# Performance work log

Measured on AMD Instinct MI355X. Metric: run time of the kernel, lower is better.

Reference implementation:

```python
import jax, jax.numpy as jnp
import numpy as np

B, T, D, H, DFF = 64, 100, 1024, 16, 4096
HD = D // H
EPS = 1e-5


def _rope_tables(t_len, hd, dtype):
    # matches RotaryEmbedding: inv_freq over even dims, emb = cat([freqs, freqs])
    inv_freq = 1.0 / (10000.0 ** (jnp.arange(0, hd, 2, dtype=jnp.float32) / hd))
    t = jnp.arange(t_len, dtype=jnp.float32)
    freqs = jnp.einsum('i,j->ij', t, inv_freq)          # (T, hd/2)
    emb = jnp.concatenate([freqs, freqs], axis=-1)      # (T, hd)
    # apply_rope uses cos[..., ::2] / sin[..., ::2]
    cos = jnp.cos(emb)[:, ::2].astype(dtype)            # (T, hd/2)
    sin = jnp.sin(emb)[:, ::2].astype(dtype)
    return cos, sin


def _apply_rope(x, cos, sin):
    # x: (B, H, T, hd); cos/sin: (T, hd/2) broadcast over B,H
    x1 = x[..., ::2]
    x2 = x[..., 1::2]
    return jnp.concatenate([x1 * cos - x2 * sin, x1 * sin + x2 * cos], axis=-1)


def _layernorm(x, g, b):
    mu = jnp.mean(x, axis=-1, keepdims=True)
    var = jnp.mean(jnp.square(x - mu), axis=-1, keepdims=True)
    return (x - mu) * jax.lax.rsqrt(var + EPS) * g + b


def setup_inputs() -> dict:
    key = jax.random.key(0)
    ks = jax.random.split(key, 8)
    s = 0.02
    return {
        'tgt': jax.random.normal(ks[0], (B, T, D), dtype=jnp.float32),
        'Wqkv': jax.random.normal(ks[1], (3 * D, D), dtype=jnp.float32) * s,
        'bqkv': jnp.zeros((3 * D,), jnp.float32),
        'Wo': jax.random.normal(ks[2], (D, D), dtype=jnp.float32) * s,
        'bo': jnp.zeros((D,), jnp.float32),
        'W1': jax.random.normal(ks[3], (DFF, D), dtype=jnp.float32) * s,
        'b1': jnp.zeros((DFF,), jnp.float32),
        'W2': jax.random.normal(ks[4], (D, DFF), dtype=jnp.float32) * s,
        'b2': jnp.zeros((D,), jnp.float32),
        'g1': jnp.ones((D,), jnp.float32),
        'be1': jnp.zeros((D,), jnp.float32),
        'g2': jnp.ones((D,), jnp.float32),
        'be2': jnp.zeros((D,), jnp.float32),
        'tgt_mask': jnp.tril(jnp.ones((T, T), jnp.int32)),
    }


def reference(tgt, Wqkv, bqkv, Wo, bo, W1, b1, W2, b2, g1, be1, g2, be2, tgt_mask):
    dtype = tgt.dtype
    # QKV projection (torch Linear: x @ W.T + b)
    qkv = jnp.einsum('btd,ed->bte', tgt, Wqkv) + bqkv          # (B,T,3D)
    qkv = qkv.reshape(B, T, 3, H, HD).transpose(2, 0, 3, 1, 4)  # (3,B,H,T,hd)
    q, k, v = qkv[0], qkv[1], qkv[2]

    cos, sin = _rope_tables(T, HD, dtype)
    q = _apply_rope(q, cos, sin)
    k = _apply_rope(k, cos, sin)

    scale = 1.0 / np.sqrt(HD)
    scores = jnp.einsum('bhqd,bhkd->bhqk', q, k) * scale        # (B,H,T,T)
    scores = jnp.where(tgt_mask == 0, -jnp.inf, scores)
    attn = jax.nn.softmax(scores, axis=-1)
    ctx = jnp.einsum('bhqk,bhkd->bhqd', attn, v)                # (B,H,T,hd)
    ctx = ctx.transpose(0, 2, 1, 3).reshape(B, T, D)

    tgt2 = jnp.einsum('btd,ed->bte', ctx, Wo) + bo
    x = _layernorm(tgt + tgt2, g1, be1)

    h = jax.nn.relu(jnp.einsum('btd,fd->btf', x, W1) + b1)
    ff = jnp.einsum('btf,df->btd', h, W2) + b2
    out = _layernorm(x + ff, g2, be2)
    return out
```

## Files before the change

### kernel.cpp

```cpp
#include <hip/hip_runtime.h>
#include <math.h>

#define Bn   64
#define Tn   100
#define Tp   128
#define Dn   1024
#define Hn   16
#define HDn  64
#define DFFn 4096
#define EPSf 1e-5f

typedef unsigned short ushort_t;
typedef __attribute__((ext_vector_type(8))) __bf16 bf16x8;
typedef __attribute__((ext_vector_type(4))) float f32x4;

__device__ __forceinline__ float u2f(ushort_t u) {
    union { unsigned int i; float f; } v; v.i = ((unsigned int)u) << 16; return v.f;
}
__device__ __forceinline__ ushort_t f2bf(float f) {
    union { float f; unsigned int u; } v; v.f = f;
    unsigned int r = v.u + 0x7FFFu + ((v.u >> 16) & 1u);
    return (ushort_t)(r >> 16);
}

__device__ __forceinline__ void gload_lds16(const void* g, void* l) {
    __builtin_amdgcn_global_load_lds(
        (const __attribute__((address_space(1))) unsigned int*)g,
        (__attribute__((address_space(3))) unsigned int*)l,
        16, 0, 0);
}

struct ConvSeg { const float* src; ushort_t* dst; int n4; };
struct Conv5   { ConvSeg seg[5]; };

__global__ __launch_bounds__(256) void conv_bf16_multi(Conv5 cfg)
{
    int i = blockIdx.x * 256 + threadIdx.x;
    #pragma unroll
    for (int s = 0; s < 5; ++s) {
        const int n = cfg.seg[s].n4;
        if (i < n) {
            float4 v = ((const float4*)cfg.seg[s].src)[i];
            ushort4 o;
            o.x = f2bf(v.x); o.y = f2bf(v.y); o.z = f2bf(v.z); o.w = f2bf(v.w);
            ((ushort4*)cfg.seg[s].dst)[i] = o;
            return;
        }
        i -= n;
    }
}

#define GEMM_TILE_MAP(gx_, gy_)                                              \
    const int L  = blockIdx.x;                                               \
    const int group = L / (8 * (gx_));                                       \
    int l = L - group * 8 * (gx_);                                           \
    const int rem = (gy_) - group * 8;                                       \
    int rowt, colt;                                                          \
    if (rem >= 8) { rowt = group * 8 + (l & 7); colt = l >> 3; }             \
    else          { rowt = group * 8 + l % rem; colt = l / rem; }

#define GEMM_KLOOP(A_, B_, K_)                                               \
    for (int k0 = 0; k0 < (K_); k0 += 64) {                                  \
        __syncthreads();                                                     \
        _Pragma("unroll")                                                    \
        for (int t = 0; t < 4; ++t) {                                        \
            const int idx = (wave * 4 + t) * 64 + lane;                      \
            const int row = idx >> 3;                                        \
            const int gc  = (idx & 7) ^ (row & 7);                           \
            gload_lds16((A_) + (size_t)(row0 + row) * (K_) + k0 + gc * 8,    \
                        &As[idx * 8]);                                       \
            gload_lds16((B_) + (size_t)(col0 + row) * (K_) + k0 + gc * 8,    \
                        &Bs[idx * 8]);                                       \
        }                                                                    \
        __syncthreads();                                                     \
        _Pragma("unroll")                                                    \
        for (int kh = 0; kh < 2; ++kh) {                                     \
            const int chunk = kh * 4 + g;                                    \
            bf16x8 af[4], bfr[4];                                            \
            _Pragma("unroll")                                                \
            for (int i = 0; i < 4; ++i) {                                    \
                const int ra = wrow + i * 16 + frow;                         \
                af[i]  = *(const bf16x8*)&As[ra * 64 + (chunk ^ (ra & 7)) * 8]; \
                const int rb = wcol + i * 16 + frow;                         \
                bfr[i] = *(const bf16x8*)&Bs[rb * 64 + (chunk ^ (rb & 7)) * 8]; \
            }                                                                \
            _Pragma("unroll")                                                \
            for (int i = 0; i < 4; ++i)                                      \
                _Pragma("unroll")                                            \
                for (int j = 0; j < 4; ++j)                                  \
                    acc[i][j] = __builtin_amdgcn_mfma_f32_16x16x32_bf16(     \
                        af[i], bfr[j], acc[i][j], 0, 0, 0);                  \
        }                                                                    \
    }

template<bool RELU, typename OutT>
__global__ __launch_bounds__(256) void gemm_bt_mfma(const ushort_t* __restrict__ A,
                                                    const ushort_t* __restrict__ Bm,
                                                    const float* __restrict__ bias,
                                                    OutT* __restrict__ C,
                                                    int M, int N, int K, int gx)
{
    __shared__ __align__(16) ushort_t As[128 * 64];
    __shared__ __align__(16) ushort_t Bs[128 * 64];

    const int gy = M >> 7;
    GEMM_TILE_MAP(gx, gy)

    const int tid  = threadIdx.x;
    const int wave = tid >> 6;
    const int lane = tid & 63;
    const int row0 = rowt * 128;
    const int col0 = colt * 128;
    const int wrow = (wave >> 1) * 64;
    const int wcol = (wave & 1) * 64;
    const int frow = lane & 15;
    const int g    = lane >> 4;

    f32x4 acc[4][4] = {};
    GEMM_KLOOP(A, Bm, K)

    const int crow = (lane >> 4) * 4;
    const int ccol = lane & 15;
    #pragma unroll
    for (int i = 0; i < 4; ++i) {
        #pragma unroll
        for (int r = 0; r < 4; ++r) {
            const int row = row0 + wrow + i * 16 + crow + r;
            #pragma unroll
            for (int j = 0; j < 4; ++j) {
                const int col = col0 + wcol + j * 16 + ccol;
                float v = acc[i][j][r] + bias[col];
                if (RELU) v = fmaxf(v, 0.f);
                if constexpr (sizeof(OutT) == 2)
                    C[(size_t)row * N + col] = (OutT)f2bf(v);
                else
                    C[(size_t)row * N + col] = (OutT)v;
            }
        }
    }
}

__global__ __launch_bounds__(256) void gemm_qkv_rope(const ushort_t* __restrict__ A,
                                                     const ushort_t* __restrict__ Bm,
                                                     const float* __restrict__ bias,
                                                     ushort_t* __restrict__ q,
                                                     ushort_t* __restrict__ k,
                                                     ushort_t* __restrict__ vt)
{
    __shared__ __align__(16) ushort_t As[128 * 64];
    __shared__ __align__(16) ushort_t Bs[128 * 64];

    const int gy = 50, gx = 24;
    GEMM_TILE_MAP(gx, gy)

    const int tid  = threadIdx.x;
    const int wave = tid >> 6;
    const int lane = tid & 63;
    const int row0 = rowt * 128;
    const int col0 = colt * 128;
    const int wrow = (wave >> 1) * 64;
    const int wcol = (wave & 1) * 64;
    const int frow = lane & 15;
    const int g    = lane >> 4;

    f32x4 acc[4][4] = {};
    GEMM_KLOOP(A, Bm, Dn)

    const int crow = (lane >> 4) * 4;
    const int ccol = lane & 15;
    const int sec  = col0 >> 10;

    if (sec == 2) {
        #pragma unroll
        for (int i = 0; i < 4; ++i) {
            #pragma unroll
            for (int r = 0; r < 4; ++r) {
                const int row = row0 + wrow + i * 16 + crow + r;
                const int b = row / Tn, t = row - b * Tn;
                #pragma unroll
                for (int j = 0; j < 4; ++j) {
                    const int colg = col0 + wcol + j * 16 + ccol;
                    const int hcol = colg & 1023;
                    const int h = hcol >> 6, d = hcol & 63;
                    const float v = acc[i][j][r] + bias[colg];
                    vt[((size_t)(b * Hn + h) * HDn + d) * Tp + t] = f2bf(v);
                }
            }
        }
    } else {
        ushort_t* dst = sec ? k : q;
        const int odd = ccol & 1;
        const float fr0 = exp2f(-0.83048202f * (float)(ccol >> 1));
        const float fr1 = exp2f(-0.83048202f * (float)(8 + (ccol >> 1)));
        #pragma unroll
        for (int i = 0; i < 4; ++i) {
            #pragma unroll
            for (int r = 0; r < 4; ++r) {
                const int row = row0 + wrow + i * 16 + crow + r;
                const int b = row / Tn, t = row - b * Tn;
                float s0, c0, s1, c1;
                sincosf((float)t * fr0, &s0, &c0);
                sincosf((float)t * fr1, &s1, &c1);
                #pragma unroll
                for (int j = 0; j < 4; ++j) {
                    const int colg = col0 + wcol + j * 16 + ccol;
                    const int hcol = colg & 1023;
                    const int h  = hcol >> 6;
                    const int dh = hcol & 63;
                    const int m  = dh >> 1;
                    const float val   = acc[i][j][r] + bias[colg];
                    const float other = __shfl_xor(val, 1);
                    const float sn = (j & 1) ? s1 : s0;
                    const float cs = (j & 1) ? c1 : c0;
                    const float x1 = odd ? other : val;
                    const float x2 = odd ? val : other;
                    const float o  = odd ? (x1 * sn + x2 * cs)
                                         : (x1 * cs - x2 * sn);
                    const int outcol = odd ? (m + 32) : m;
                    dst[((size_t)(b * Hn + h) * Tp + t) * HDn + outcol] = f2bf(o);
                }
            }
        }
    }
}

__global__ __launch_bounds__(256) void attn_mfma(const ushort_t* __restrict__ q,
                                                 const ushort_t* __restrict__ k,
                                                 const ushort_t* __restrict__ vt,
                                                 ushort_t* __restrict__ ctx)
{
    __shared__ __align__(16) ushort_t sm[24576];

    const int bh   = blockIdx.x;
    const int b    = bh >> 4, h = bh & 15;
    const int tid  = threadIdx.x;
    const int wave = tid >> 6;
    const int lane = tid & 63;
    const int c    = lane & 15;
    const int g    = lane >> 4;
    const int R0   = wave * 32;

    const ushort_t* qg = q  + (size_t)bh * Tp * HDn;
    const ushort_t* kg = k  + (size_t)bh * Tp * HDn;
    const ushort_t* vg = vt + (size_t)bh * HDn * Tp;
    for (int s = wave; s < 16; s += 4) {
        const int idx = s * 64 + lane;
        { const int row = idx >> 3, pc = idx & 7, gc = pc ^ (row & 7);
          gload_lds16(qg + row * 64 + gc * 8, &sm[idx * 8]);
          gload_lds16(kg + row * 64 + gc * 8, &sm[8192 + idx * 8]); }
        { const int row = idx >> 4, pc = idx & 15, gc = pc ^ (row & 15);
          gload_lds16(vg + row * 128 + gc * 8, &sm[16384 + idx * 8]); }
    }
    __syncthreads();

    f32x4 acc[2][8] = {};
    #pragma unroll
    for (int ks = 0; ks < 2; ++ks) {
        const int cb = ks * 4;
        bf16x8 aq[2];
        #pragma unroll
        for (int i = 0; i < 2; ++i) {
            const int row = R0 + i * 16 + c;
            const int ph  = (cb + g) ^ (row & 7);
            aq[i] = *(const bf16x8*)&sm[row * 64 + ph * 8];
        }
        #pragma unroll
        for (int j = 0; j < 8; ++j) {
            const int row = j * 16 + c;
            const int ph  = (cb + g) ^ (row & 7);
            const bf16x8 bk = *(const bf16x8*)&sm[8192 + row * 64 + ph * 8];
            acc[0][j] = __builtin_amdgcn_mfma_f32_16x16x32_bf16(aq[0], bk, acc[0][j], 0, 0, 0);
            acc[1][j] = __builtin_amdgcn_mfma_f32_16x16x32_bf16(aq[1], bk, acc[1][j], 0, 0, 0);
        }
    }
    __syncthreads();

    float linv[2][4];
    #pragma unroll
    for (int i = 0; i < 2; ++i) {
        #pragma unroll
        for (int r = 0; r < 4; ++r) {
            const int row = R0 + i * 16 + g * 4 + r;
            float sv[8], m = -1e30f;
            #pragma unroll
            for (int j = 0; j < 8; ++j) {
                const int col = j * 16 + c;
                const float s = acc[i][j][r] * 0.125f;
                sv[j] = (col <= row) ? s : -1e30f;
                m = fmaxf(m, sv[j]);
            }
            #pragma unroll
            for (int msk = 1; msk < 16; msk <<= 1) m = fmaxf(m, __shfl_xor(m, msk));
            float l = 0.f;
            #pragma unroll
            for (int j = 0; j < 8; ++j) {
                const int col = j * 16 + c;
                const float p = (col <= row) ? __expf(sv[j] - m) : 0.f;
                sv[j] = p; l += p;
            }
            #pragma unroll
            for (int msk = 1; msk < 16; msk <<= 1) l += __shfl_xor(l, msk);
            linv[i][r] = 1.f / l;
            #pragma unroll
            for (int j = 0; j < 8; ++j) {
                const int chunk = j * 2 + (c >> 3);
                const int ph    = chunk ^ (row & 15);
                sm[row * 128 + ph * 8 + (c & 7)] = f2bf(sv[j]);
            }
        }
    }
    __syncthreads();

    f32x4 acc2[2][4] = {};
    #pragma unroll
    for (int ks = 0; ks < 4; ++ks) {
        const int cb = ks * 4;
        bf16x8 ap[2];
        #pragma unroll
        for (int i = 0; i < 2; ++i) {
            const int row = R0 + i * 16 + c;
            const int ph  = (cb + g) ^ (row & 15);
            ap[i] = *(const bf16x8*)&sm[row * 128 + ph * 8];
        }
        #pragma unroll
        for (int n = 0; n < 4; ++n) {
            const int row = n * 16 + c;
            const int ph  = (cb + g) ^ (row & 15);
            const bf16x8 bv = *(const bf16x8*)&sm[16384 + row * 128 + ph * 8];
            acc2[0][n] = __builtin_amdgcn_mfma_f32_16x16x32_bf16(ap[0], bv, acc2[0][n], 0, 0, 0);
            acc2[1][n] = __builtin_amdgcn_mfma_f32_16x16x32_bf16(ap[1], bv, acc2[1][n], 0, 0, 0);
        }
    }

    #pragma unroll
    for (int i = 0; i < 2; ++i) {
        #pragma unroll
        for (int r = 0; r < 4; ++r) {
            const int row = R0 + i * 16 + g * 4 + r;
            if (row < Tn) {
                const float s = linv[i][r];
                #pragma unroll
                for (int n = 0; n < 4; ++n) {
                    const int col = n * 16 + c;
                    ctx[(size_t)(b * Tn + row) * Dn + h * HDn + col] =
                        f2bf(acc2[i][n][r] * s);
                }
            }
        }
    }
}

__global__ __launch_bounds__(256) void add_ln1(const float* __restrict__ a,
                                               const ushort_t* __restrict__ r,
                                               const float* __restrict__ g,
                                               const float* __restrict__ be,
                                               ushort_t* __restrict__ out_bf)
{
    const int row = blockIdx.x;
    const int tid = threadIdx.x;
    __shared__ float red[256];
    const size_t base = (size_t)row * Dn;

    float vals[4];
    float s = 0.f;
    #pragma unroll
    for (int i = 0; i < 4; ++i) {
        const int c = tid + i * 256;
        vals[i] = a[base + c] + u2f(r[base + c]);
        s += vals[i];
    }
    red[tid] = s;
    __syncthreads();
    for (int o = 128; o > 0; o >>= 1) {
        if (tid < o) red[tid] += red[tid + o];
        __syncthreads();
    }
    const float mu = red[0] * (1.f / Dn);
    __syncthreads();

    float vs = 0.f;
    #pragma unroll
    for (int i = 0; i < 4; ++i) { const float d = vals[i] - mu; vs += d * d; }
    red[tid] = vs;
    __syncthreads();
    for (int o = 128; o > 0; o >>= 1) {
        if (tid < o) red[tid] += red[tid + o];
        __syncthreads();
    }
    const float rstd = rsqrtf(red[0] * (1.f / Dn) + EPSf);

    #pragma unroll
    for (int i = 0; i < 4; ++i) {
        const int c = tid + i * 256;
        out_bf[base + c] = f2bf((vals[i] - mu) * rstd * g[c] + be[c]);
    }
}

__global__ __launch_bounds__(256) void add_ln2(const ushort_t* __restrict__ a,
                                               const ushort_t* __restrict__ r,
                                               const float* __restrict__ g,
                                               const float* __restrict__ be,
                                               float* __restrict__ out)
{
    const int row = blockIdx.x;
    const int tid = threadIdx.x;
    __shared__ float red[256];
    const size_t base = (size_t)row * Dn;

    float vals[4];
    float s = 0.f;
    #pragma unroll
    for (int i = 0; i < 4; ++i) {
        const int c = tid + i * 256;
        vals[i] = u2f(a[base + c]) + u2f(r[base + c]);
        s += vals[i];
    }
    red[tid] = s;
    __syncthreads();
    for (int o = 128; o > 0; o >>= 1) {
        if (tid < o) red[tid] += red[tid + o];
        __syncthreads();
    }
    const float mu = red[0] * (1.f / Dn);
    __syncthreads();

    float vs = 0.f;
    #pragma unroll
    for (int i = 0; i < 4; ++i) { const float d = vals[i] - mu; vs += d * d; }
    red[tid] = vs;
    __syncthreads();
    for (int o = 128; o > 0; o >>= 1) {
        if (tid < o) red[tid] += red[tid + o];
        __syncthreads();
    }
    const float rstd = rsqrtf(red[0] * (1.f / Dn) + EPSf);

    #pragma unroll
    for (int i = 0; i < 4; ++i) {
        const int c = tid + i * 256;
        out[base + c] = (vals[i] - mu) * rstd * g[c] + be[c];
    }
}

extern "C" void kernel_launch(void* const* d_in, const int* in_sizes, int n_in,
                              void* d_out, int out_size, void* d_ws, size_t ws_size,
                              hipStream_t stream)
{
    const float* tgt  = (const float*)d_in[0];
    const float* Wqkv = (const float*)d_in[1];
    const float* bqkv = (const float*)d_in[2];
    const float* Wo   = (const float*)d_in[3];
    const float* bo   = (const float*)d_in[4];
    const float* W1   = (const float*)d_in[5];
    const float* b1   = (const float*)d_in[6];
    const float* W2   = (const float*)d_in[7];
    const float* b2   = (const float*)d_in[8];
    const float* g1   = (const float*)d_in[9];
    const float* be1  = (const float*)d_in[10];
    const float* g2   = (const float*)d_in[11];
    const float* be2  = (const float*)d_in[12];
    float* out = (float*)d_out;
    (void)in_sizes; (void)n_in; (void)out_size; (void)ws_size;

    const int M = Bn * Tn;

    char* w = (char*)d_ws;
    ushort_t* tgt_bf  = (ushort_t*)(w);
    ushort_t* Wqkv_bf = (ushort_t*)(w + 13107200);
    ushort_t* Wo_bf   = (ushort_t*)(w + 19398656);
    ushort_t* W1_bf   = (ushort_t*)(w + 21495808);
    ushort_t* W2_bf   = (ushort_t*)(w + 29884416);

    ushort_t* qb    = (ushort_t*)(w + 38273024);
    ushort_t* kb    = (ushort_t*)(w + 55050240);
    ushort_t* vtb   = (ushort_t*)(w + 71827456);
    ushort_t* hbuf  = (ushort_t*)(w + 38273024);
    ushort_t* ctxb  = (ushort_t*)(w + 88604672);
    ushort_t* tgt2b = (ushort_t*)(w + 101711872);
    ushort_t* ffb   = (ushort_t*)(w + 101711872);
    ushort_t* x_bf  = (ushort_t*)(w + 114819072);

    Conv5 cfg;
    cfg.seg[0] = { tgt,  tgt_bf,  M * Dn / 4 };
    cfg.seg[1] = { Wqkv, Wqkv_bf, 3 * Dn * Dn / 4 };
    cfg.seg[2] = { Wo,   Wo_bf,   Dn * Dn / 4 };
    cfg.seg[3] = { W1,   W1_bf,   DFFn * Dn / 4 };
    cfg.seg[4] = { W2,   W2_bf,   Dn * DFFn / 4 };
    const int total4 = (M * Dn + 3 * Dn * Dn + Dn * Dn + 2 * DFFn * Dn) / 4;
    conv_bf16_multi<<<(total4 + 255) / 256, 256, 0, stream>>>(cfg);

    gemm_qkv_rope<<<1200, 256, 0, stream>>>(tgt_bf, Wqkv_bf, bqkv, qb, kb, vtb);
    attn_mfma<<<Bn * Hn, 256, 0, stream>>>(qb, kb, vtb, ctxb);
    gemm_bt_mfma<false, ushort_t><<<(Dn / 128) * (M / 128), 256, 0, stream>>>(
        ctxb, Wo_bf, bo, tgt2b, M, Dn, Dn, Dn / 128);
    add_ln1<<<M, 256, 0, stream>>>(tgt, tgt2b, g1, be1, x_bf);
    gemm_bt_mfma<true, ushort_t><<<(DFFn / 128) * (M / 128), 256, 0, stream>>>(
        x_bf, W1_bf, b1, hbuf, M, DFFn, Dn, DFFn / 128);
    gemm_bt_mfma<false, ushort_t><<<(Dn / 128) * (M / 128), 256, 0, stream>>>(
        hbuf, W2_bf, b2, ffb, M, Dn, DFFn, Dn / 128);
    add_ln2<<<M, 256, 0, stream>>>(x_bf, ffb, g2, be2, out);
}
```

Measured before the change: 450.9 us.

## Fuse residual into Wo GEMM, precompute RoPE table, toggle tile swizzle

The Wo GEMM epilogue now adds the residual, reading the bf16 copy of tgt, and layernorm1 becomes a single-input kernel, so the fp32 tgt read moves out of the LN pass. The QKV GEMM epilogue builds a per-block cos/sin table in shared memory, which removes the sincosf calls repeated across j and lanes. The tile swizzle becomes switchable and is turned off for the W1 GEMM. The residual now comes from bf16-rounded tgt rather than fp32, which slightly changes accuracy, and rounding tgt2 to bf16 after the add loses some precision.

```diff
diff --git a/kernel.cpp b/kernel.cpp
--- a/kernel.cpp
+++ b/kernel.cpp
@@ -50,14 +50,16 @@
     }
 }
 
-#define GEMM_TILE_MAP(gx_, gy_)                                              \
+#define GEMM_TILE_MAP(gx_, gy_, swz_)                                        \
     const int L  = blockIdx.x;                                               \
-    const int group = L / (8 * (gx_));                                       \
-    int l = L - group * 8 * (gx_);                                           \
-    const int rem = (gy_) - group * 8;                                       \
     int rowt, colt;                                                          \
-    if (rem >= 8) { rowt = group * 8 + (l & 7); colt = l >> 3; }             \
-    else          { rowt = group * 8 + l % rem; colt = l / rem; }
+    if (swz_) {                                                              \
+        const int group = L / (8 * (gx_));                                   \
+        int l = L - group * 8 * (gx_);                                       \
+        const int rem = (gy_) - group * 8;                                   \
+        if (rem >= 8) { rowt = group * 8 + (l & 7); colt = l >> 3; }         \
+        else          { rowt = group * 8 + l % rem; colt = l / rem; }        \
+    } else { rowt = L / (gx_); colt = L - rowt * (gx_); }
 
 #define GEMM_KLOOP(A_, B_, K_)                                               \
     for (int k0 = 0; k0 < (K_); k0 += 64) {                                  \
@@ -93,18 +95,20 @@
         }                                                                    \
     }
 
-template<bool RELU, typename OutT>
+template<bool RELU, bool ADDRES, typename OutT>
 __global__ __launch_bounds__(256) void gemm_bt_mfma(const ushort_t* __restrict__ A,
                                                     const ushort_t* __restrict__ Bm,
                                                     const float* __restrict__ bias,
+                                                    const ushort_t* __restrict__ res,
                                                     OutT* __restrict__ C,
-                                                    int M, int N, int K, int gx)
+                                                    int M, int N, int K,
+                                                    int gx, int swz)
 {
     __shared__ __align__(16) ushort_t As[128 * 64];
     __shared__ __align__(16) ushort_t Bs[128 * 64];
 
     const int gy = M >> 7;
-    GEMM_TILE_MAP(gx, gy)
+    GEMM_TILE_MAP(gx, gy, swz)
 
     const int tid  = threadIdx.x;
     const int wave = tid >> 6;
@@ -130,6 +134,7 @@
             for (int j = 0; j < 4; ++j) {
                 const int col = col0 + wcol + j * 16 + ccol;
                 float v = acc[i][j][r] + bias[col];
+                if (ADDRES) v += u2f(res[(size_t)row * N + col]);
                 if (RELU) v = fmaxf(v, 0.f);
                 if constexpr (sizeof(OutT) == 2)
                     C[(size_t)row * N + col] = (OutT)f2bf(v);
@@ -151,7 +156,7 @@
     __shared__ __align__(16) ushort_t Bs[128 * 64];
 
     const int gy = 50, gx = 24;
-    GEMM_TILE_MAP(gx, gy)
+    GEMM_TILE_MAP(gx, gy, 1)
 
     const int tid  = threadIdx.x;
     const int wave = tid >> 6;
@@ -166,9 +171,25 @@
     f32x4 acc[4][4] = {};
     GEMM_KLOOP(A, Bm, Dn)
 
+    const int sec = col0 >> 10;
+
+    __syncthreads();
+    float2* tab = (float2*)As;
+    if (sec != 2) {
+        for (int e = tid; e < 2048; e += 256) {
+            const int lr = e >> 4, f = e & 15;
+            const int row = row0 + lr;
+            const int b = row / Tn;
+            const int t = row - b * Tn;
+            float s, c;
+            sincosf((float)t * exp2f(-0.83048202f * (float)f), &s, &c);
+            tab[lr * 16 + f] = make_float2(c, s);
+        }
+    }
+    __syncthreads();
+
     const int crow = (lane >> 4) * 4;
     const int ccol = lane & 15;
-    const int sec  = col0 >> 10;
 
     if (sec == 2) {
         #pragma unroll
@@ -190,17 +211,17 @@
     } else {
         ushort_t* dst = sec ? k : q;
         const int odd = ccol & 1;
-        const float fr0 = exp2f(-0.83048202f * (float)(ccol >> 1));
-        const float fr1 = exp2f(-0.83048202f * (float)(8 + (ccol >> 1)));
+        const int f0  = ccol >> 1;
         #pragma unroll
         for (int i = 0; i < 4; ++i) {
             #pragma unroll
             for (int r = 0; r < 4; ++r) {
-                const int row = row0 + wrow + i * 16 + crow + r;
+                const int lr  = wrow + i * 16 + crow + r;
+                const int row = row0 + lr;
                 const int b = row / Tn, t = row - b * Tn;
-                float s0, c0, s1, c1;
-                sincosf((float)t * fr0, &s0, &c0);
-                sincosf((float)t * fr1, &s1, &c1);
+                const float2 cs0 = tab[lr * 16 + f0];
+                const float2 cs1 = tab[lr * 16 + 8 + f0];
+                (void)t;
                 #pragma unroll
                 for (int j = 0; j < 4; ++j) {
                     const int colg = col0 + wcol + j * 16 + ccol;
@@ -210,8 +231,8 @@
                     const int m  = dh >> 1;
                     const float val   = acc[i][j][r] + bias[colg];
                     const float other = __shfl_xor(val, 1);
-                    const float sn = (j & 1) ? s1 : s0;
-                    const float cs = (j & 1) ? c1 : c0;
+                    const float sn = (j & 1) ? cs1.y : cs0.y;
+                    const float cs = (j & 1) ? cs1.x : cs0.x;
                     const float x1 = odd ? other : val;
                     const float x2 = odd ? val : other;
                     const float o  = odd ? (x1 * sn + x2 * cs)
@@ -350,11 +371,10 @@
     }
 }
 
-__global__ __launch_bounds__(256) void add_ln1(const float* __restrict__ a,
-                                               const ushort_t* __restrict__ r,
-                                               const float* __restrict__ g,
-                                               const float* __restrict__ be,
-                                               ushort_t* __restrict__ out_bf)
+__global__ __launch_bounds__(256) void ln_single(const ushort_t* __restrict__ a,
+                                                 const float* __restrict__ g,
+                                                 const float* __restrict__ be,
+                                                 ushort_t* __restrict__ out_bf)
 {
     const int row = blockIdx.x;
     const int tid = threadIdx.x;
@@ -366,7 +386,7 @@
     #pragma unroll
     for (int i = 0; i < 4; ++i) {
         const int c = tid + i * 256;
-        vals[i] = a[base + c] + u2f(r[base + c]);
+        vals[i] = u2f(a[base + c]);
         s += vals[i];
     }
     red[tid] = s;
@@ -491,12 +511,12 @@
 
     gemm_qkv_rope<<<1200, 256, 0, stream>>>(tgt_bf, Wqkv_bf, bqkv, qb, kb, vtb);
     attn_mfma<<<Bn * Hn, 256, 0, stream>>>(qb, kb, vtb, ctxb);
-    gemm_bt_mfma<false, ushort_t><<<(Dn / 128) * (M / 128), 256, 0, stream>>>(
-        ctxb, Wo_bf, bo, tgt2b, M, Dn, Dn, Dn / 128);
-    add_ln1<<<M, 256, 0, stream>>>(tgt, tgt2b, g1, be1, x_bf);
-    gemm_bt_mfma<true, ushort_t><<<(DFFn / 128) * (M / 128), 256, 0, stream>>>(
-        x_bf, W1_bf, b1, hbuf, M, DFFn, Dn, DFFn / 128);
-    gemm_bt_mfma<false, ushort_t><<<(Dn / 128) * (M / 128), 256, 0, stream>>>(
-        hbuf, W2_bf, b2, ffb, M, Dn, DFFn, Dn / 128);
+    gemm_bt_mfma<false, true, ushort_t><<<(Dn / 128) * (M / 128), 256, 0, stream>>>(
+        ctxb, Wo_bf, bo, tgt_bf, tgt2b, M, Dn, Dn, Dn / 128, 1);
+    ln_single<<<M, 256, 0, stream>>>(tgt2b, g1, be1, x_bf);
+    gemm_bt_mfma<true, false, ushort_t><<<(DFFn / 128) * (M / 128), 256, 0, stream>>>(
+        x_bf, W1_bf, b1, nullptr, hbuf, M, DFFn, Dn, DFFn / 128, 0);
+    gemm_bt_mfma<false, false, ushort_t><<<(Dn / 128) * (M / 128), 256, 0, stream>>>(
+        hbuf, W2_bf, b2, nullptr, ffb, M, Dn, DFFn, Dn / 128, 1);
     add_ln2<<<M, 256, 0, stream>>>(x_bf, ffb, g2, be2, out);
 }
```

Measured after the change: 436.6 us. 3.2% less time.
